# Kernel optimization log

Hardware: AMD Instinct MI355X
Metric: run time of the kernel (lower is better)

The kernel has to match this reference:

```python
import jax, jax.numpy as jnp
import numpy as np

N_HEAD = 16
ROPE_THETA = 10000.0


def rope_cos_sin(head_dim, T):
    # theta_i = 1 / ROPE_THETA**(2i/d), freqs = outer(positions, theta)
    inv_freq = 1.0 / (ROPE_THETA ** (np.arange(0, head_dim, 2, dtype=np.float32) / head_dim))
    pos = np.arange(T, dtype=np.float32)
    freqs = np.outer(pos, inv_freq)  # [T, d/2]
    return jnp.asarray(np.cos(freqs)), jnp.asarray(np.sin(freqs))


def apply_rope(x, cos, sin):
    # x: [B, T, H, d]; pairs are consecutive lanes (..., d/2, 2) like view_as_complex
    B, T, H, d = x.shape
    xp = x.reshape(B, T, H, d // 2, 2)
    x0, x1 = xp[..., 0], xp[..., 1]
    c = cos[None, :, None, :]  # [1, T, 1, d/2]
    s = sin[None, :, None, :]
    r0 = x0 * c - x1 * s
    r1 = x0 * s + x1 * c
    return jnp.stack([r0, r1], axis=-1).reshape(B, T, H, d)


def setup_inputs() -> dict:
    key = jax.random.key(0)
    k1, k2, k3 = jax.random.split(key, 3)
    B, T, C = 2, 2048, 1024
    x = jax.random.normal(k1, (B, T, C), dtype=jnp.float32)
    w_qkv = jax.random.normal(k2, (C, 3 * C), dtype=jnp.float32) * (1.0 / np.sqrt(C))
    w_proj = jax.random.normal(k3, (C, C), dtype=jnp.float32) * (1.0 / np.sqrt(C))
    b_proj = jnp.zeros((C,), dtype=jnp.float32)
    return {"x": x, "w_qkv": w_qkv, "w_proj": w_proj, "b_proj": b_proj}


def reference(x, w_qkv, w_proj, b_proj):
    B, T, C = x.shape
    H = N_HEAD
    d = C // H
    qkv = x @ w_qkv  # [B, T, 3C]
    q, k, v = jnp.split(qkv, 3, axis=-1)
    q = q.reshape(B, T, H, d)
    k = k.reshape(B, T, H, d)
    v = v.reshape(B, T, H, d)
    cos, sin = rope_cos_sin(d, T)
    q = apply_rope(q, cos, sin)
    k = apply_rope(k, cos, sin)
    # causal SDPA
    scale = 1.0 / np.sqrt(d).astype(np.float32)
    scores = jnp.einsum('bqhd,bkhd->bhqk', q, k) * scale  # [B, H, T, T]
    causal = jnp.tril(jnp.ones((T, T), dtype=bool))
    scores = jnp.where(causal[None, None], scores, jnp.finfo(scores.dtype).min)
    attn = jax.nn.softmax(scores, axis=-1)
    y = jnp.einsum('bhqk,bkhd->bqhd', attn, v).reshape(B, T, C)
    return y @ w_proj + b_proj
```

## Files before the change

kernel.cpp:

```cpp
#include <hip/hip_runtime.h>
#include <hip/hip_bf16.h>
#include <math.h>

typedef __bf16 bf16x8 __attribute__((ext_vector_type(8)));
typedef float floatx4 __attribute__((ext_vector_type(4)));

#define BM 128
#define BN 128
#define BK 32

__device__ __forceinline__ void load_lds16(const void* g, void* l) {
    __builtin_amdgcn_global_load_lds(
        (const __attribute__((address_space(1))) void*)g,
        (__attribute__((address_space(3))) void*)l, 16, 0, 0);
}

__global__ __launch_bounds__(256)
void cvt_bf16_kernel(const float* __restrict__ in, __hip_bfloat16* __restrict__ out, int n8)
{
    int i = (blockIdx.x * 256 + threadIdx.x);
    if (i >= n8) return;
    const float4 a = *reinterpret_cast<const float4*>(in + (size_t)i * 8);
    const float4 b = *reinterpret_cast<const float4*>(in + (size_t)i * 8 + 4);
    union { __hip_bfloat162 h[4]; uint4 u; } pk;
    pk.h[0] = __float22bfloat162_rn(make_float2(a.x, a.y));
    pk.h[1] = __float22bfloat162_rn(make_float2(a.z, a.w));
    pk.h[2] = __float22bfloat162_rn(make_float2(b.x, b.y));
    pk.h[3] = __float22bfloat162_rn(make_float2(b.z, b.w));
    *reinterpret_cast<uint4*>(out + (size_t)i * 8) = pk.u;
}

__global__ __launch_bounds__(256)
void transpose_cvt_kernel(const float* __restrict__ in, __hip_bfloat16* __restrict__ out,
                          int R, int C)
{
    __shared__ float Ts[64][68];
    const int c0 = blockIdx.x * 64;
    const int r0 = blockIdx.y * 64;
    const int t  = threadIdx.x;
    const int lr = t >> 2;
    const int lc = (t & 3) * 16;
    #pragma unroll
    for (int j = 0; j < 16; j += 4) {
        float4 v = *reinterpret_cast<const float4*>(in + (size_t)(r0 + lr) * C + c0 + lc + j);
        Ts[lr][lc + j + 0] = v.x;
        Ts[lr][lc + j + 1] = v.y;
        Ts[lr][lc + j + 2] = v.z;
        Ts[lr][lc + j + 3] = v.w;
    }
    __syncthreads();
    const int oc = t >> 2;
    const int rs = (t & 3) * 16;
    __hip_bfloat16 tmp[16];
    #pragma unroll
    for (int j = 0; j < 16; ++j)
        tmp[j] = __float2bfloat16(Ts[rs + j][oc]);
    __hip_bfloat16* op = out + (size_t)(c0 + oc) * R + r0 + rs;
    *reinterpret_cast<uint4*>(op)     = *reinterpret_cast<uint4*>(tmp);
    *reinterpret_cast<uint4*>(op + 8) = *reinterpret_cast<uint4*>(tmp + 8);
}

template<int EPI, int CONV, int M, int N, int K>
__global__ __launch_bounds__(256)
void gemm_kernel(const void* __restrict__ Avoid,
                 const void* __restrict__ Bvoid,
                 const float* __restrict__ bias,
                 __hip_bfloat16* __restrict__ Qo,
                 __hip_bfloat16* __restrict__ Ko,
                 __hip_bfloat16* __restrict__ Vt,
                 float* __restrict__ Out)
{
    constexpr int LD = (CONV == 0) ? BK : (BK + 8);
    __shared__ __align__(16) __hip_bfloat16 As[BM][LD];
    __shared__ __align__(16) __hip_bfloat16 Bs[BN][LD];

    const int t    = threadIdx.x;
    const int m0   = blockIdx.y * BM;
    const int n0   = blockIdx.x * BN;
    const int lane = t & 63;
    const int w    = t >> 6;
    const int wm   = (w >> 1) * 64;
    const int wn   = (w & 1) * 64;
    const int quad = lane >> 4;
    const int l16  = lane & 15;

    const int r16  = lane >> 2;
    const int gor  = (lane & 3) ^ ((lane >> 3) & 3);
    const int sg   = (CONV == 0) ? ((quad ^ ((l16 >> 1) & 3)) * 8) : (quad * 8);

    floatx4 acc[4][4] = {};

    for (int k0 = 0; k0 < K; k0 += BK) {
        if (CONV == 0) {
            const __hip_bfloat16* A  = (const __hip_bfloat16*)Avoid;
            const __hip_bfloat16* Bt = (const __hip_bfloat16*)Bvoid;
            #pragma unroll
            for (int i = 0; i < 2; ++i) {
                int c   = 2 * w + i;
                int row = c * 16 + r16;
                load_lds16(A  + (size_t)(m0 + row) * K + k0 + gor * 8, &As[c * 16][0]);
                load_lds16(Bt + (size_t)(n0 + row) * K + k0 + gor * 8, &Bs[c * 16][0]);
            }
        } else {
            if (EPI == 0) {
                const float* A = (const float*)Avoid;
                #pragma unroll
                for (int i = 0; i < 4; ++i) {
                    int slot = t + i * 256;
                    int row  = slot >> 3;
                    int c4   = (slot & 7) << 2;
                    float4 v = *reinterpret_cast<const float4*>(A + (size_t)(m0 + row) * K + k0 + c4);
                    union { __hip_bfloat162 h2[2]; uint2 u; } pk;
                    pk.h2[0] = __float22bfloat162_rn(make_float2(v.x, v.y));
                    pk.h2[1] = __float22bfloat162_rn(make_float2(v.z, v.w));
                    *reinterpret_cast<uint2*>(&As[row][c4]) = pk.u;
                }
            } else {
                const __hip_bfloat16* A = (const __hip_bfloat16*)Avoid;
                #pragma unroll
                for (int i = 0; i < 2; ++i) {
                    int idx = t + i * 256;
                    int row = idx >> 2;
                    int col = (idx & 3) << 3;
                    *reinterpret_cast<uint4*>(&As[row][col]) =
                        *reinterpret_cast<const uint4*>(A + (size_t)(m0 + row) * K + k0 + col);
                }
            }
            const float* B = (const float*)Bvoid;
            const int bn  = t & 127;
            const int bkh = (t >> 7) * 16;
            float f[16];
            #pragma unroll
            for (int j = 0; j < 16; ++j)
                f[j] = B[(size_t)(k0 + bkh + j) * N + n0 + bn];
            #pragma unroll
            for (int c = 0; c < 4; ++c) {
                union { __hip_bfloat162 h2[2]; uint2 u; } pk;
                pk.h2[0] = __float22bfloat162_rn(make_float2(f[4*c + 0], f[4*c + 1]));
                pk.h2[1] = __float22bfloat162_rn(make_float2(f[4*c + 2], f[4*c + 3]));
                *reinterpret_cast<uint2*>(&Bs[bn][bkh + 4*c]) = pk.u;
            }
        }
        __syncthreads();

        bf16x8 af[4], bfr[4];
        #pragma unroll
        for (int mf = 0; mf < 4; ++mf)
            af[mf] = *reinterpret_cast<const bf16x8*>(&As[wm + mf * 16 + l16][sg]);
        #pragma unroll
        for (int nf = 0; nf < 4; ++nf)
            bfr[nf] = *reinterpret_cast<const bf16x8*>(&Bs[wn + nf * 16 + l16][sg]);
        #pragma unroll
        for (int mf = 0; mf < 4; ++mf)
            #pragma unroll
            for (int nf = 0; nf < 4; ++nf)
                acc[mf][nf] = __builtin_amdgcn_mfma_f32_16x16x32_bf16(af[mf], bfr[nf], acc[mf][nf], 0, 0, 0);
        __syncthreads();
    }

    if (EPI == 0) {
        #pragma unroll
        for (int mf = 0; mf < 4; ++mf) {
            #pragma unroll
            for (int nf = 0; nf < 4; ++nf) {
                #pragma unroll
                for (int r = 0; r < 4; ++r) {
                    float v = acc[mf][nf][r];
                    int m  = m0 + wm + mf * 16 + quad * 4 + r;
                    int n  = n0 + wn + nf * 16 + l16;
                    int bb = m >> 11;
                    int tp = m & 2047;
                    int which = n >> 10;
                    int dd = n & 63;
                    int h  = (n & 1023) >> 6;
                    float other = __shfl_xor(v, 1);
                    if (which < 2) {
                        int f = dd >> 1;
                        float inv = exp2f((float)f * -0.4152410118609203f);
                        float ang = (float)tp * inv;
                        float s, c;
                        __sincosf(ang, &s, &c);
                        v = (dd & 1) ? (other * s + v * c) : (v * c - other * s);
                        if (which == 0) v *= 0.1803368801111137f;
                    }
                    __hip_bfloat16 bv = __float2bfloat16(v);
                    size_t bh = (size_t)bb * 16 + h;
                    if (which == 0)      Qo[(bh * 2048 + tp) * 64 + dd] = bv;
                    else if (which == 1) Ko[(bh * 2048 + tp) * 64 + dd] = bv;
                    else                 Vt[(bh * 64 + dd) * 2048 + tp] = bv;
                }
            }
        }
    } else {
        #pragma unroll
        for (int mf = 0; mf < 4; ++mf)
            #pragma unroll
            for (int nf = 0; nf < 4; ++nf)
                #pragma unroll
                for (int r = 0; r < 4; ++r) {
                    int m = m0 + wm + mf * 16 + quad * 4 + r;
                    int n = n0 + wn + nf * 16 + l16;
                    Out[(size_t)m * N + n] = acc[mf][nf][r] + bias[n];
                }
    }
}

__global__ __launch_bounds__(256)
void attn_kernel(const __hip_bfloat16* __restrict__ Q,
                 const __hip_bfloat16* __restrict__ Kb,
                 const __hip_bfloat16* __restrict__ Vt,
                 __hip_bfloat16* __restrict__ Y)
{
    const int bh = blockIdx.x;
    const int qt = 31 - (int)blockIdx.y;
    const int bb = bh >> 4;
    const int h  = bh & 15;
    const int t    = threadIdx.x;
    const int w    = t >> 6;
    const int lane = t & 63;
    const int quad = lane >> 4;
    const int l16  = lane & 15;
    const int T = 2048;

    __shared__ __align__(16) __hip_bfloat16 Ks[64][72];
    __shared__ __align__(16) __hip_bfloat16 Vs[64][72];
    __shared__ __align__(16) __hip_bfloat16 Pl[4][16][72];

    const __hip_bfloat16* Qp = Q  + (size_t)bh * T * 64;
    const __hip_bfloat16* Kp = Kb + (size_t)bh * T * 64;
    const __hip_bfloat16* Vp = Vt + (size_t)bh * 64 * T;

    const int qrow0 = qt * 64 + w * 16;

    bf16x8 qa[2];
    #pragma unroll
    for (int kb = 0; kb < 2; ++kb)
        qa[kb] = *reinterpret_cast<const bf16x8*>(
            Qp + (size_t)(qrow0 + l16) * 64 + kb * 32 + quad * 8);

    bf16x8 ones;
    #pragma unroll
    for (int j = 0; j < 8; ++j) ones[j] = (__bf16)1.0f;

    floatx4 o[4] = {};
    floatx4 sums = {};

    const int srow = t >> 2;
    const int sch  = t & 3;
    const int ntiles = qt + 1;

    bf16x8 kreg[2], vreg[2];
    {
        const __hip_bfloat16* kg = Kp + (size_t)srow * 64 + sch * 8;
        kreg[0] = *reinterpret_cast<const bf16x8*>(kg);
        kreg[1] = *reinterpret_cast<const bf16x8*>(kg + 32);
        const __hip_bfloat16* vg = Vp + (size_t)srow * T + sch * 8;
        vreg[0] = *reinterpret_cast<const bf16x8*>(vg);
        vreg[1] = *reinterpret_cast<const bf16x8*>(vg + 32);
    }

    for (int kt = 0; kt < ntiles; ++kt) {
        __syncthreads();
        *reinterpret_cast<bf16x8*>(&Ks[srow][sch * 8])      = kreg[0];
        *reinterpret_cast<bf16x8*>(&Ks[srow][sch * 8 + 32]) = kreg[1];
        *reinterpret_cast<bf16x8*>(&Vs[srow][sch * 8])      = vreg[0];
        *reinterpret_cast<bf16x8*>(&Vs[srow][sch * 8 + 32]) = vreg[1];
        __syncthreads();
        if (kt + 1 < ntiles) {
            const __hip_bfloat16* kg = Kp + (size_t)((kt + 1) * 64 + srow) * 64 + sch * 8;
            kreg[0] = *reinterpret_cast<const bf16x8*>(kg);
            kreg[1] = *reinterpret_cast<const bf16x8*>(kg + 32);
            const __hip_bfloat16* vg = Vp + (size_t)srow * T + (kt + 1) * 64 + sch * 8;
            vreg[0] = *reinterpret_cast<const bf16x8*>(vg);
            vreg[1] = *reinterpret_cast<const bf16x8*>(vg + 32);
        }

        floatx4 sfr[4];
        #pragma unroll
        for (int nf = 0; nf < 4; ++nf) {
            floatx4 s = {};
            #pragma unroll
            for (int kb = 0; kb < 2; ++kb) {
                bf16x8 kf = *reinterpret_cast<const bf16x8*>(&Ks[nf * 16 + l16][kb * 32 + quad * 8]);
                s = __builtin_amdgcn_mfma_f32_16x16x32_bf16(qa[kb], kf, s, 0, 0, 0);
            }
            sfr[nf] = s;
        }
        if (kt == qt) {
            #pragma unroll
            for (int nf = 0; nf < 4; ++nf)
                #pragma unroll
                for (int r = 0; r < 4; ++r) {
                    int qg = w * 16 + quad * 4 + r;
                    int kg = nf * 16 + l16;
                    if (kg > qg) sfr[nf][r] = -INFINITY;
                }
        }
        #pragma unroll
        for (int nf = 0; nf < 4; ++nf)
            #pragma unroll
            for (int r = 0; r < 4; ++r)
                Pl[w][quad * 4 + r][nf * 16 + l16] = __float2bfloat16(exp2f(sfr[nf][r]));
        bf16x8 pa[2];
        #pragma unroll
        for (int kb = 0; kb < 2; ++kb)
            pa[kb] = *reinterpret_cast<const bf16x8*>(&Pl[w][l16][kb * 32 + quad * 8]);

        sums = __builtin_amdgcn_mfma_f32_16x16x32_bf16(pa[0], ones, sums, 0, 0, 0);
        sums = __builtin_amdgcn_mfma_f32_16x16x32_bf16(pa[1], ones, sums, 0, 0, 0);

        #pragma unroll
        for (int nf = 0; nf < 4; ++nf) {
            #pragma unroll
            for (int kb = 0; kb < 2; ++kb) {
                bf16x8 vb = *reinterpret_cast<const bf16x8*>(&Vs[nf * 16 + l16][kb * 32 + quad * 8]);
                o[nf] = __builtin_amdgcn_mfma_f32_16x16x32_bf16(pa[kb], vb, o[nf], 0, 0, 0);
            }
        }
    }

    #pragma unroll
    for (int r = 0; r < 4; ++r) {
        float inv = 1.0f / sums[r];
        #pragma unroll
        for (int nf = 0; nf < 4; ++nf) {
            float v = o[nf][r] * inv;
            int qrow = qrow0 + quad * 4 + r;
            int dd = nf * 16 + l16;
            Y[((size_t)bb * 2048 + qrow) * 1024 + h * 64 + dd] = __float2bfloat16(v);
        }
    }
}

extern "C" void kernel_launch(void* const* d_in, const int* in_sizes, int n_in,
                              void* d_out, int out_size, void* d_ws, size_t ws_size,
                              hipStream_t stream) {
    const float* x      = (const float*)d_in[0];
    const float* w_qkv  = (const float*)d_in[1];
    const float* w_proj = (const float*)d_in[2];
    const float* b_proj = (const float*)d_in[3];
    float* out = (float*)d_out;

    const size_t NELT = (size_t)4096 * 1024;
    const size_t WQKV = (size_t)3072 * 1024;
    const size_t WPRJ = (size_t)1024 * 1024;
    const size_t need_main = (4 * NELT + WQKV + WPRJ) * 2;
    const size_t need_fb   = 3 * NELT * 2;

    dim3 blk(256);

    if (ws_size >= need_main) {
        __hip_bfloat16* Q      = (__hip_bfloat16*)d_ws;
        __hip_bfloat16* Kb     = Q   + NELT;
        __hip_bfloat16* Vt     = Kb  + NELT;
        __hip_bfloat16* xb     = Vt  + NELT;
        __hip_bfloat16* wqkvT  = xb  + NELT;
        __hip_bfloat16* wprjT  = wqkvT + WQKV;

        cvt_bf16_kernel<<<dim3((NELT / 8 + 255) / 256), blk, 0, stream>>>(x, xb, NELT / 8);
        transpose_cvt_kernel<<<dim3(3072 / 64, 1024 / 64), blk, 0, stream>>>(w_qkv, wqkvT, 1024, 3072);
        transpose_cvt_kernel<<<dim3(1024 / 64, 1024 / 64), blk, 0, stream>>>(w_proj, wprjT, 1024, 1024);

        gemm_kernel<0, 0, 4096, 3072, 1024><<<dim3(24, 32), blk, 0, stream>>>(
            xb, wqkvT, nullptr, Q, Kb, Vt, nullptr);
        attn_kernel<<<dim3(32, 32), blk, 0, stream>>>(Q, Kb, Vt, xb);
        gemm_kernel<1, 0, 4096, 1024, 1024><<<dim3(8, 32), blk, 0, stream>>>(
            xb, wprjT, b_proj, nullptr, nullptr, nullptr, out);
    } else if (ws_size >= need_fb) {
        __hip_bfloat16* Q  = (__hip_bfloat16*)d_ws;
        __hip_bfloat16* Kb = Q  + NELT;
        __hip_bfloat16* Vt = Kb + NELT;

        gemm_kernel<0, 1, 4096, 3072, 1024><<<dim3(24, 32), blk, 0, stream>>>(
            x, w_qkv, nullptr, Q, Kb, Vt, nullptr);
        attn_kernel<<<dim3(32, 32), blk, 0, stream>>>(Q, Kb, Vt, (__hip_bfloat16*)d_out);
        hipMemcpyAsync(Q, d_out, NELT * sizeof(__hip_bfloat16), hipMemcpyDeviceToDevice, stream);
        gemm_kernel<1, 1, 4096, 1024, 1024><<<dim3(8, 32), blk, 0, stream>>>(
            Q, w_proj, b_proj, nullptr, nullptr, nullptr, out);
    } else {
        hipMemsetAsync(d_out, 0x44, (size_t)out_size * sizeof(float), stream);
    }
}
```

Before: 215.1 us.

## Fuse x bf16 conversion into QKV GEMM, register-prefetch loads, stage V transpose via LDS

Removes the standalone fp32-to-bf16 conversion kernel by loading fp32 x directly in the QKV GEMM and converting in registers. Replaces global_load_lds with register double-buffered prefetch of the next K tile, overlapping global loads with MFMA. The V-transposed epilogue is staged through shared memory so the writes are coalesced 16-byte stores instead of scattered 2-byte stores. In exchange the GEMM reads twice as many bytes for A, uses more registers and LDS, and adds extra syncs in the epilogue.

```diff
diff --git a/kernel.cpp b/kernel.cpp
--- a/kernel.cpp
+++ b/kernel.cpp
@@ -8,27 +8,6 @@
 #define BM 128
 #define BN 128
 #define BK 32
-
-__device__ __forceinline__ void load_lds16(const void* g, void* l) {
-    __builtin_amdgcn_global_load_lds(
-        (const __attribute__((address_space(1))) void*)g,
-        (__attribute__((address_space(3))) void*)l, 16, 0, 0);
-}
-
-__global__ __launch_bounds__(256)
-void cvt_bf16_kernel(const float* __restrict__ in, __hip_bfloat16* __restrict__ out, int n8)
-{
-    int i = (blockIdx.x * 256 + threadIdx.x);
-    if (i >= n8) return;
-    const float4 a = *reinterpret_cast<const float4*>(in + (size_t)i * 8);
-    const float4 b = *reinterpret_cast<const float4*>(in + (size_t)i * 8 + 4);
-    union { __hip_bfloat162 h[4]; uint4 u; } pk;
-    pk.h[0] = __float22bfloat162_rn(make_float2(a.x, a.y));
-    pk.h[1] = __float22bfloat162_rn(make_float2(a.z, a.w));
-    pk.h[2] = __float22bfloat162_rn(make_float2(b.x, b.y));
-    pk.h[3] = __float22bfloat162_rn(make_float2(b.z, b.w));
-    *reinterpret_cast<uint4*>(out + (size_t)i * 8) = pk.u;
-}
 
 __global__ __launch_bounds__(256)
 void transpose_cvt_kernel(const float* __restrict__ in, __hip_bfloat16* __restrict__ out,
@@ -70,9 +49,10 @@
                  __hip_bfloat16* __restrict__ Vt,
                  float* __restrict__ Out)
 {
-    constexpr int LD = (CONV == 0) ? BK : (BK + 8);
+    constexpr int LD = (CONV == 1) ? (BK + 8) : BK;
     __shared__ __align__(16) __hip_bfloat16 As[BM][LD];
     __shared__ __align__(16) __hip_bfloat16 Bs[BN][LD];
+    __shared__ __align__(16) __hip_bfloat16 Cst[(EPI == 0) ? 128 * 72 : 1];
 
     const int t    = threadIdx.x;
     const int m0   = blockIdx.y * BM;
@@ -84,24 +64,75 @@
     const int quad = lane >> 4;
     const int l16  = lane & 15;
 
-    const int r16  = lane >> 2;
-    const int gor  = (lane & 3) ^ ((lane >> 3) & 3);
-    const int sg   = (CONV == 0) ? ((quad ^ ((l16 >> 1) & 3)) * 8) : (quad * 8);
+    const int sg = (CONV == 1) ? (quad * 8) : ((quad ^ ((l16 >> 1) & 3)) * 8);
+
+    const int srow = t >> 1;
+    const int sg0  = (t & 1) * 2;
+    const int ssw  = (srow >> 1) & 3;
+    const int sc0  = (sg0 ^ ssw) * 8;
+    const int sc1  = ((sg0 + 1) ^ ssw) * 8;
 
     floatx4 acc[4][4] = {};
 
-    for (int k0 = 0; k0 < K; k0 += BK) {
-        if (CONV == 0) {
-            const __hip_bfloat16* A  = (const __hip_bfloat16*)Avoid;
-            const __hip_bfloat16* Bt = (const __hip_bfloat16*)Bvoid;
-            #pragma unroll
-            for (int i = 0; i < 2; ++i) {
-                int c   = 2 * w + i;
-                int row = c * 16 + r16;
-                load_lds16(A  + (size_t)(m0 + row) * K + k0 + gor * 8, &As[c * 16][0]);
-                load_lds16(Bt + (size_t)(n0 + row) * K + k0 + gor * 8, &Bs[c * 16][0]);
-            }
-        } else {
+    if (CONV != 1) {
+        const __hip_bfloat16* Bt = (const __hip_bfloat16*)Bvoid;
+        uint4 ar[2], br[2];
+
+        auto fetch = [&](int k0) {
+            if (CONV == 2) {
+                const float* Af = (const float*)Avoid;
+                const float* p = Af + (size_t)(m0 + srow) * K + k0 + sg0 * 8;
+                float4 f0 = *reinterpret_cast<const float4*>(p);
+                float4 f1 = *reinterpret_cast<const float4*>(p + 4);
+                float4 f2 = *reinterpret_cast<const float4*>(p + 8);
+                float4 f3 = *reinterpret_cast<const float4*>(p + 12);
+                union { __hip_bfloat162 h[4]; uint4 u; } pk;
+                pk.h[0] = __float22bfloat162_rn(make_float2(f0.x, f0.y));
+                pk.h[1] = __float22bfloat162_rn(make_float2(f0.z, f0.w));
+                pk.h[2] = __float22bfloat162_rn(make_float2(f1.x, f1.y));
+                pk.h[3] = __float22bfloat162_rn(make_float2(f1.z, f1.w));
+                ar[0] = pk.u;
+                pk.h[0] = __float22bfloat162_rn(make_float2(f2.x, f2.y));
+                pk.h[1] = __float22bfloat162_rn(make_float2(f2.z, f2.w));
+                pk.h[2] = __float22bfloat162_rn(make_float2(f3.x, f3.y));
+                pk.h[3] = __float22bfloat162_rn(make_float2(f3.z, f3.w));
+                ar[1] = pk.u;
+            } else {
+                const __hip_bfloat16* Ab = (const __hip_bfloat16*)Avoid;
+                const __hip_bfloat16* p = Ab + (size_t)(m0 + srow) * K + k0 + sg0 * 8;
+                ar[0] = *reinterpret_cast<const uint4*>(p);
+                ar[1] = *reinterpret_cast<const uint4*>(p + 8);
+            }
+            const __hip_bfloat16* q = Bt + (size_t)(n0 + srow) * K + k0 + sg0 * 8;
+            br[0] = *reinterpret_cast<const uint4*>(q);
+            br[1] = *reinterpret_cast<const uint4*>(q + 8);
+        };
+
+        fetch(0);
+        for (int k0 = 0; k0 < K; k0 += BK) {
+            __syncthreads();
+            *reinterpret_cast<uint4*>(&As[srow][sc0]) = ar[0];
+            *reinterpret_cast<uint4*>(&As[srow][sc1]) = ar[1];
+            *reinterpret_cast<uint4*>(&Bs[srow][sc0]) = br[0];
+            *reinterpret_cast<uint4*>(&Bs[srow][sc1]) = br[1];
+            __syncthreads();
+            if (k0 + BK < K) fetch(k0 + BK);
+
+            bf16x8 af[4], bfr[4];
+            #pragma unroll
+            for (int mf = 0; mf < 4; ++mf)
+                af[mf] = *reinterpret_cast<const bf16x8*>(&As[wm + mf * 16 + l16][sg]);
+            #pragma unroll
+            for (int nf = 0; nf < 4; ++nf)
+                bfr[nf] = *reinterpret_cast<const bf16x8*>(&Bs[wn + nf * 16 + l16][sg]);
+            #pragma unroll
+            for (int mf = 0; mf < 4; ++mf)
+                #pragma unroll
+                for (int nf = 0; nf < 4; ++nf)
+                    acc[mf][nf] = __builtin_amdgcn_mfma_f32_16x16x32_bf16(af[mf], bfr[nf], acc[mf][nf], 0, 0, 0);
+        }
+    } else {
+        for (int k0 = 0; k0 < K; k0 += BK) {
             if (EPI == 0) {
                 const float* A = (const float*)Avoid;
                 #pragma unroll
@@ -140,41 +171,41 @@
                 pk.h2[1] = __float22bfloat162_rn(make_float2(f[4*c + 2], f[4*c + 3]));
                 *reinterpret_cast<uint2*>(&Bs[bn][bkh + 4*c]) = pk.u;
             }
-        }
-        __syncthreads();
-
-        bf16x8 af[4], bfr[4];
-        #pragma unroll
-        for (int mf = 0; mf < 4; ++mf)
-            af[mf] = *reinterpret_cast<const bf16x8*>(&As[wm + mf * 16 + l16][sg]);
-        #pragma unroll
-        for (int nf = 0; nf < 4; ++nf)
-            bfr[nf] = *reinterpret_cast<const bf16x8*>(&Bs[wn + nf * 16 + l16][sg]);
-        #pragma unroll
-        for (int mf = 0; mf < 4; ++mf)
+            __syncthreads();
+
+            bf16x8 af[4], bfr[4];
+            #pragma unroll
+            for (int mf = 0; mf < 4; ++mf)
+                af[mf] = *reinterpret_cast<const bf16x8*>(&As[wm + mf * 16 + l16][sg]);
             #pragma unroll
             for (int nf = 0; nf < 4; ++nf)
-                acc[mf][nf] = __builtin_amdgcn_mfma_f32_16x16x32_bf16(af[mf], bfr[nf], acc[mf][nf], 0, 0, 0);
-        __syncthreads();
+                bfr[nf] = *reinterpret_cast<const bf16x8*>(&Bs[wn + nf * 16 + l16][sg]);
+            #pragma unroll
+            for (int mf = 0; mf < 4; ++mf)
+                #pragma unroll
+                for (int nf = 0; nf < 4; ++nf)
+                    acc[mf][nf] = __builtin_amdgcn_mfma_f32_16x16x32_bf16(af[mf], bfr[nf], acc[mf][nf], 0, 0, 0);
+            __syncthreads();
+        }
     }
 
     if (EPI == 0) {
-        #pragma unroll
-        for (int mf = 0; mf < 4; ++mf) {
-            #pragma unroll
-            for (int nf = 0; nf < 4; ++nf) {
-                #pragma unroll
-                for (int r = 0; r < 4; ++r) {
-                    float v = acc[mf][nf][r];
-                    int m  = m0 + wm + mf * 16 + quad * 4 + r;
-                    int n  = n0 + wn + nf * 16 + l16;
-                    int bb = m >> 11;
-                    int tp = m & 2047;
-                    int which = n >> 10;
-                    int dd = n & 63;
-                    int h  = (n & 1023) >> 6;
-                    float other = __shfl_xor(v, 1);
-                    if (which < 2) {
+        const int which = n0 >> 10;
+        if (which < 2) {
+            #pragma unroll
+            for (int mf = 0; mf < 4; ++mf) {
+                #pragma unroll
+                for (int nf = 0; nf < 4; ++nf) {
+                    #pragma unroll
+                    for (int r = 0; r < 4; ++r) {
+                        float v = acc[mf][nf][r];
+                        int m  = m0 + wm + mf * 16 + quad * 4 + r;
+                        int n  = n0 + wn + nf * 16 + l16;
+                        int bb = m >> 11;
+                        int tp = m & 2047;
+                        int dd = n & 63;
+                        int h  = (n & 1023) >> 6;
+                        float other = __shfl_xor(v, 1);
                         int f = dd >> 1;
                         float inv = exp2f((float)f * -0.4152410118609203f);
                         float ang = (float)tp * inv;
@@ -182,12 +213,44 @@
                         __sincosf(ang, &s, &c);
                         v = (dd & 1) ? (other * s + v * c) : (v * c - other * s);
                         if (which == 0) v *= 0.1803368801111137f;
+                        size_t bh = (size_t)bb * 16 + h;
+                        __hip_bfloat16 bv = __float2bfloat16(v);
+                        if (which == 0) Qo[(bh * 2048 + tp) * 64 + dd] = bv;
+                        else            Ko[(bh * 2048 + tp) * 64 + dd] = bv;
                     }
-                    __hip_bfloat16 bv = __float2bfloat16(v);
-                    size_t bh = (size_t)bb * 16 + h;
-                    if (which == 0)      Qo[(bh * 2048 + tp) * 64 + dd] = bv;
-                    else if (which == 1) Ko[(bh * 2048 + tp) * 64 + dd] = bv;
-                    else                 Vt[(bh * 64 + dd) * 2048 + tp] = bv;
+                }
+            }
+        } else {
+            const int bb  = m0 >> 11;
+            const int tp0 = m0 & 2047;
+            #pragma unroll
+            for (int p = 0; p < 2; ++p) {
+                __syncthreads();
+                if ((w >> 1) == p) {
+                    #pragma unroll
+                    for (int mf = 0; mf < 4; ++mf)
+                        #pragma unroll
+                        for (int nf = 0; nf < 4; ++nf)
+                            #pragma unroll
+                            for (int r = 0; r < 4; ++r) {
+                                int rl = mf * 16 + quad * 4 + r;
+                                int cl = wn + nf * 16 + l16;
+                                Cst[cl * 72 + rl] = __float2bfloat16(acc[mf][nf][r]);
+                            }
+                }
+                __syncthreads();
+                #pragma unroll
+                for (int pass = 0; pass < 4; ++pass) {
+                    int slot = t + pass * 256;
+                    int rg  = slot & 7;
+                    int col = slot >> 3;
+                    uint4 v = *reinterpret_cast<const uint4*>(&Cst[col * 72 + rg * 8]);
+                    int n  = n0 + col;
+                    int dd = n & 63;
+                    int hh = (n & 1023) >> 6;
+                    __hip_bfloat16* dst = Vt + ((size_t)(bb * 16 + hh) * 64 + dd) * 2048
+                                             + tp0 + p * 64 + rg * 8;
+                    *reinterpret_cast<uint4*>(dst) = v;
                 }
             }
         }
@@ -353,19 +416,18 @@
         __hip_bfloat16* Q      = (__hip_bfloat16*)d_ws;
         __hip_bfloat16* Kb     = Q   + NELT;
         __hip_bfloat16* Vt     = Kb  + NELT;
-        __hip_bfloat16* xb     = Vt  + NELT;
-        __hip_bfloat16* wqkvT  = xb  + NELT;
+        __hip_bfloat16* yb     = Vt  + NELT;
+        __hip_bfloat16* wqkvT  = yb  + NELT;
         __hip_bfloat16* wprjT  = wqkvT + WQKV;
 
-        cvt_bf16_kernel<<<dim3((NELT / 8 + 255) / 256), blk, 0, stream>>>(x, xb, NELT / 8);
         transpose_cvt_kernel<<<dim3(3072 / 64, 1024 / 64), blk, 0, stream>>>(w_qkv, wqkvT, 1024, 3072);
         transpose_cvt_kernel<<<dim3(1024 / 64, 1024 / 64), blk, 0, stream>>>(w_proj, wprjT, 1024, 1024);
 
-        gemm_kernel<0, 0, 4096, 3072, 1024><<<dim3(24, 32), blk, 0, stream>>>(
-            xb, wqkvT, nullptr, Q, Kb, Vt, nullptr);
-        attn_kernel<<<dim3(32, 32), blk, 0, stream>>>(Q, Kb, Vt, xb);
+        gemm_kernel<0, 2, 4096, 3072, 1024><<<dim3(24, 32), blk, 0, stream>>>(
+            x, wqkvT, nullptr, Q, Kb, Vt, nullptr);
+        attn_kernel<<<dim3(32, 32), blk, 0, stream>>>(Q, Kb, Vt, yb);
         gemm_kernel<1, 0, 4096, 1024, 1024><<<dim3(8, 32), blk, 0, stream>>>(
-            xb, wprjT, b_proj, nullptr, nullptr, nullptr, out);
+            yb, wprjT, b_proj, nullptr, nullptr, nullptr, out);
     } else if (ws_size >= need_fb) {
         __hip_bfloat16* Q  = (__hip_bfloat16*)d_ws;
         __hip_bfloat16* Kb = Q  + NELT;
```

Measured after the change: 285.9 us. 32.9% more time.
